# Kernel tuning notes

Hardware: AMD Instinct MI355X
Metric: run time of the kernel (lower is better)

## Reference

```python
import jax, jax.numpy as jnp
import numpy as np


def setup_inputs() -> dict:
    key = jax.random.key(0)
    ka, kb = jax.random.split(key)
    a = jax.random.normal(ka, (8, 2048, 1024), dtype=jnp.float32)
    b = jax.random.normal(kb, (8, 2048, 1024), dtype=jnp.float32)
    return {"a": a, "b": b}


def reference(a, b):
    # e[b,i,j] = <a_i, b_j>
    e = jnp.einsum("bid,bjd->bij", a, b)  # [B, La, Lb]
    e_b = jax.nn.softmax(e, axis=2)        # softmax over b-tokens
    e_a = jax.nn.softmax(e, axis=1)        # softmax over a-tokens
    a_tilda = jnp.einsum("bij,bjd->bid", e_b, b)  # [B, La, D]
    b_tilda = jnp.einsum("bij,bid->bjd", e_a, a)  # [B, Lb, D]
    return (a_tilda, b_tilda)
```

## Files before the change

kernel.cpp:

```cpp
#include <hip/hip_runtime.h>

#define BATCH 8
#define L 2048
#define D 1024

#define PB_OFF  (L * L)
#define PAT_OFF (L * L + (L * L) / 2)
#define STAT    (2 * L * L)
#define ROWINV  0
#define CMAXP   (L)
#define CMAX    (17 * L)
#define CSUMP   (18 * L)
#define CINV    (26 * L)
#define SLOT_F  (2 * L * L + 28 * L)

typedef __attribute__((ext_vector_type(8))) short bf16x8;
typedef __attribute__((ext_vector_type(4))) float f32x4;

static __device__ inline unsigned short f2bf(float x) {
  union { float f; unsigned u; } v; v.f = x;
  unsigned r = v.u + 0x7fff + ((v.u >> 16) & 1);
  return (unsigned short)(r >> 16);
}
static __device__ inline float bf2f(unsigned short h) {
  union { unsigned u; float f; } v; v.u = ((unsigned)h) << 16; return v.f;
}
static __device__ inline unsigned pack2(float x, float y) {
  return (unsigned)f2bf(x) | ((unsigned)f2bf(y) << 16);
}
static __device__ inline void split2(float x, float y, unsigned &hi, unsigned &lo) {
  unsigned short hx = f2bf(x), hy = f2bf(y);
  float rx = x - bf2f(hx), ry = y - bf2f(hy);
  hi = (unsigned)hx | ((unsigned)hy << 16);
  lo = (unsigned)f2bf(rx) | ((unsigned)f2bf(ry) << 16);
}

#define GLL16(gp, lp) __builtin_amdgcn_global_load_lds(                        \
    (const __attribute__((address_space(1))) void*)(gp),                       \
    (__attribute__((address_space(3))) void*)(lp), 16, 0, 0)

static __device__ inline void stage2(const unsigned short* __restrict__ g,
                                     size_t o0, size_t o1,
                                     unsigned short* l, int wb) {
  GLL16(g + o0, l + wb);
  GLL16(g + o1, l + wb + 2048);
}

__global__ __launch_bounds__(256) void k_prep(const float* __restrict__ A,
                                              const float* __restrict__ Bm,
                                              unsigned short* __restrict__ at,
                                              unsigned short* __restrict__ bt,
                                              unsigned short* __restrict__ ah,
                                              unsigned short* __restrict__ al,
                                              unsigned short* __restrict__ bh,
                                              unsigned short* __restrict__ bl) {
  const int z = blockIdx.z, batch = z & 7;
  const bool isA = z < 8;
  const float* src = (isA ? A : Bm) + (size_t)batch * L * D;
  unsigned short* dst = (isA ? at : bt) + (size_t)batch * D * L;
  unsigned short* ph = (isA ? ah : bh) + (size_t)batch * L * D;
  unsigned short* pl = (isA ? al : bl) + (size_t)batch * L * D;
  const int i0 = blockIdx.x * 64, d0 = blockIdx.y * 64;
  __shared__ float sT[64][65];
  const int tid = threadIdx.x;
#pragma unroll
  for (int it = 0; it < 4; ++it) {
    int idx = tid + it * 256;
    int row = idx >> 4, c4 = (idx & 15) * 4;
    float4 v = *(const float4*)(src + (size_t)(i0 + row) * D + d0 + c4);
    unsigned h0, l0, h1, l1;
    split2(v.x, v.y, h0, l0); split2(v.z, v.w, h1, l1);
    size_t po = (size_t)(i0 + row) * D + d0 + c4;
    *(uint2*)&ph[po] = make_uint2(h0, h1);
    *(uint2*)&pl[po] = make_uint2(l0, l1);
    sT[row][c4 + 0] = v.x; sT[row][c4 + 1] = v.y;
    sT[row][c4 + 2] = v.z; sT[row][c4 + 3] = v.w;
  }
  __syncthreads();
#pragma unroll
  for (int it = 0; it < 4; ++it) {
    int idx = tid + it * 256;
    int orow = idx >> 4, c4 = (idx & 15) * 4;
    uint2 o = make_uint2(pack2(sT[c4 + 0][orow], sT[c4 + 1][orow]),
                         pack2(sT[c4 + 2][orow], sT[c4 + 3][orow]));
    *(uint2*)&dst[(size_t)(d0 + orow) * L + i0 + c4] = o;
  }
}

__global__ __launch_bounds__(256) void k_gemm_e(const unsigned short* __restrict__ ah,
                                                const unsigned short* __restrict__ al,
                                                const unsigned short* __restrict__ bh,
                                                const unsigned short* __restrict__ bl,
                                                float* __restrict__ ws, int b0) {
  const int bz = blockIdx.z, batch = b0 + bz;
  const size_t po = (size_t)batch * L * D;
  float* e = ws + (size_t)bz * SLOT_F;
  const int i0 = blockIdx.x * 128, j0 = blockIdx.y * 128;
  __shared__ unsigned short sAh[128 * 32], sAl[128 * 32];
  __shared__ unsigned short sBh[128 * 32], sBl[128 * 32];
  const int tid = threadIdx.x, lane = tid & 63, wave = tid >> 6;
  const int wm = (wave & 1) * 64, wn = (wave >> 1) * 64;
  const int q = lane >> 4, lr = lane & 15;
  const int soff = wave * 1024 + lane * 16;
  const int srow = soff >> 6, scol = (soff & 63) >> 1;
  const int wb = wave * 512;
  const unsigned short* gAh = ah + po; const unsigned short* gAl = al + po;
  const unsigned short* gBh = bh + po; const unsigned short* gBl = bl + po;
  const size_t ga0 = (size_t)(i0 + srow) * D + scol, ga1 = ga0 + (size_t)64 * D;
  const size_t gb0 = (size_t)(j0 + srow) * D + scol, gb1 = gb0 + (size_t)64 * D;
  f32x4 acc[4][4] = {};
  for (int k0 = 0; k0 < D; k0 += 32) {
    __syncthreads();
    stage2(gAh, ga0 + k0, ga1 + k0, sAh, wb);
    stage2(gAl, ga0 + k0, ga1 + k0, sAl, wb);
    stage2(gBh, gb0 + k0, gb1 + k0, sBh, wb);
    stage2(gBl, gb0 + k0, gb1 + k0, sBl, wb);
    __syncthreads();
    bf16x8 fah[4], fbh[4], fx[4];
#pragma unroll
    for (int t = 0; t < 4; ++t) {
      fah[t] = *(const bf16x8*)&sAh[(wm + t * 16 + lr) * 32 + q * 8];
      fbh[t] = *(const bf16x8*)&sBh[(wn + t * 16 + lr) * 32 + q * 8];
    }
#pragma unroll
    for (int mi = 0; mi < 4; ++mi)
#pragma unroll
      for (int ni = 0; ni < 4; ++ni)
        acc[mi][ni] = __builtin_amdgcn_mfma_f32_16x16x32_bf16(fah[mi], fbh[ni], acc[mi][ni], 0, 0, 0);
#pragma unroll
    for (int t = 0; t < 4; ++t)
      fx[t] = *(const bf16x8*)&sBl[(wn + t * 16 + lr) * 32 + q * 8];
#pragma unroll
    for (int mi = 0; mi < 4; ++mi)
#pragma unroll
      for (int ni = 0; ni < 4; ++ni)
        acc[mi][ni] = __builtin_amdgcn_mfma_f32_16x16x32_bf16(fah[mi], fx[ni], acc[mi][ni], 0, 0, 0);
#pragma unroll
    for (int t = 0; t < 4; ++t)
      fx[t] = *(const bf16x8*)&sAl[(wm + t * 16 + lr) * 32 + q * 8];
#pragma unroll
    for (int mi = 0; mi < 4; ++mi)
#pragma unroll
      for (int ni = 0; ni < 4; ++ni)
        acc[mi][ni] = __builtin_amdgcn_mfma_f32_16x16x32_bf16(fx[mi], fbh[ni], acc[mi][ni], 0, 0, 0);
  }
#pragma unroll
  for (int mi = 0; mi < 4; ++mi)
#pragma unroll
    for (int ni = 0; ni < 4; ++ni)
#pragma unroll
      for (int r = 0; r < 4; ++r)
        e[(size_t)(i0 + wm + mi * 16 + q * 4 + r) * L + (j0 + wn + ni * 16 + lr)] =
            acc[mi][ni][r];
}

__global__ __launch_bounds__(256) void k_rowsoft(float* __restrict__ ws) {
  float* slot = ws + (size_t)blockIdx.y * SLOT_F;
  const int row = blockIdx.x, tid = threadIdx.x;
  const float* er = slot + (size_t)row * L;
  float v[8]; float m = -INFINITY;
#pragma unroll
  for (int r = 0; r < 8; ++r) { v[r] = er[tid + r * 256]; m = fmaxf(m, v[r]); }
  __shared__ float red[4];
#pragma unroll
  for (int o = 32; o; o >>= 1) m = fmaxf(m, __shfl_xor(m, o));
  if ((tid & 63) == 0) red[tid >> 6] = m;
  __syncthreads();
  m = fmaxf(fmaxf(red[0], red[1]), fmaxf(red[2], red[3]));
  float ex[8], s = 0.f;
#pragma unroll
  for (int r = 0; r < 8; ++r) { ex[r] = __expf(v[r] - m); s += ex[r]; }
  __syncthreads();
#pragma unroll
  for (int o = 32; o; o >>= 1) s += __shfl_xor(s, o);
  if ((tid & 63) == 0) red[tid >> 6] = s;
  __syncthreads();
  unsigned short* P = (unsigned short*)(slot + PB_OFF) + (size_t)row * L;
#pragma unroll
  for (int r = 0; r < 8; ++r) P[tid + r * 256] = f2bf(ex[r]);
  if (tid == 0)
    slot[STAT + ROWINV + row] = 1.0f / (red[0] + red[1] + red[2] + red[3]);
}

__global__ __launch_bounds__(256) void k_colmax(float* __restrict__ ws) {
  float* slot = ws + (size_t)blockIdx.z * SLOT_F;
  const float* e = slot;
  float* st = slot + STAT;
  const int j0 = blockIdx.x * 64, i0 = blockIdx.y * 256;
  const int tid = threadIdx.x;
  const int rr = tid >> 4, c4 = (tid & 15) * 4;
  float m0 = -INFINITY, m1 = -INFINITY, m2 = -INFINITY, m3 = -INFINITY;
#pragma unroll 4
  for (int i = rr; i < 256; i += 16) {
    float4 v = *(const float4*)(e + (size_t)(i0 + i) * L + j0 + c4);
    m0 = fmaxf(m0, v.x); m1 = fmaxf(m1, v.y);
    m2 = fmaxf(m2, v.z); m3 = fmaxf(m3, v.w);
  }
  __shared__ float red[16][64];
  red[rr][c4 + 0] = m0; red[rr][c4 + 1] = m1;
  red[rr][c4 + 2] = m2; red[rr][c4 + 3] = m3;
  __syncthreads();
  if (tid < 64) {
    float m = red[0][tid];
#pragma unroll
    for (int g = 1; g < 16; ++g) m = fmaxf(m, red[g][tid]);
    st[CMAXP + (size_t)blockIdx.y * L + j0 + tid] = m;
  }
}

__global__ __launch_bounds__(256) void k_colstat2(float* __restrict__ ws) {
  float* st = ws + (size_t)blockIdx.y * SLOT_F + STAT;
  const int j = blockIdx.x * 256 + threadIdx.x;
  float m = st[CMAXP + j];
#pragma unroll
  for (int k = 1; k < 8; ++k) m = fmaxf(m, st[CMAXP + (size_t)k * L + j]);
  st[CMAX + j] = m;
}

__global__ __launch_bounds__(256) void k_colexp(float* __restrict__ ws) {
  float* slot = ws + (size_t)blockIdx.z * SLOT_F;
  const float* e = slot;
  float* st = slot + STAT;
  const int j0 = blockIdx.x * 64, i0 = blockIdx.y * 256;
  const int tid = threadIdx.x;
  const int rr = tid >> 4, c4 = (tid & 15) * 4;
  __shared__ unsigned short sT[64][72];
  __shared__ float psumL[16][64];
  float cm[4], ps[4] = {0.f, 0.f, 0.f, 0.f};
#pragma unroll
  for (int k = 0; k < 4; ++k) cm[k] = st[CMAX + j0 + c4 + k];
  unsigned short* PaT = (unsigned short*)(slot + PAT_OFF);
  for (int sub = 0; sub < 4; ++sub) {
    const int ib = i0 + sub * 64;
    __syncthreads();
#pragma unroll
    for (int p = 0; p < 4; ++p) {
      const int r = rr + p * 16;
      float4 v = *(const float4*)(e + (size_t)(ib + r) * L + j0 + c4);
      float e0 = __expf(v.x - cm[0]), e1 = __expf(v.y - cm[1]);
      float e2 = __expf(v.z - cm[2]), e3 = __expf(v.w - cm[3]);
      ps[0] += e0; ps[1] += e1; ps[2] += e2; ps[3] += e3;
      sT[c4 + 0][r] = f2bf(e0); sT[c4 + 1][r] = f2bf(e1);
      sT[c4 + 2][r] = f2bf(e2); sT[c4 + 3][r] = f2bf(e3);
    }
    __syncthreads();
    const int cc = tid >> 2, qd = tid & 3;
    uint4 o0 = *(const uint4*)&sT[cc][qd * 8];
    uint4 o1 = *(const uint4*)&sT[cc][32 + qd * 8];
    *(uint4*)&PaT[(size_t)(j0 + cc) * L + ib + qd * 8] = o0;
    *(uint4*)&PaT[(size_t)(j0 + cc) * L + ib + 32 + qd * 8] = o1;
  }
  psumL[rr][c4 + 0] = ps[0]; psumL[rr][c4 + 1] = ps[1];
  psumL[rr][c4 + 2] = ps[2]; psumL[rr][c4 + 3] = ps[3];
  __syncthreads();
  if (tid < 64) {
    float s = 0.f;
#pragma unroll
    for (int g = 0; g < 16; ++g) s += psumL[g][tid];
    st[CSUMP + (size_t)blockIdx.y * L + j0 + tid] = s;
  }
}

__global__ __launch_bounds__(256) void k_colfin(float* __restrict__ ws) {
  float* st = ws + (size_t)blockIdx.y * SLOT_F + STAT;
  const int j = blockIdx.x * 256 + threadIdx.x;
  float s = 0.f;
#pragma unroll
  for (int k = 0; k < 8; ++k) s += st[CSUMP + (size_t)k * L + j];
  st[CINV + j] = 1.0f / s;
}

__global__ __launch_bounds__(256) void k_pv(const unsigned short* __restrict__ at,
                                            const unsigned short* __restrict__ bt,
                                            float* __restrict__ ws,
                                            float* __restrict__ outB,
                                            int b0, int nb) {
  const int z = blockIdx.z;
  const int pair = (z >= nb) ? 1 : 0;
  const int bz = z - pair * nb;
  const int batch = b0 + bz;
  float* slot = ws + (size_t)bz * SLOT_F;
  const unsigned short* P =
      (const unsigned short*)(slot + (pair ? PAT_OFF : PB_OFF));
  const unsigned short* W = (pair ? at : bt) + (size_t)batch * D * L;
  float* out = outB + (size_t)(pair * BATCH + batch) * L * D;
  const float* sc = slot + STAT + (pair ? CINV : ROWINV);
  const int m0 = blockIdx.x * 128, d0 = blockIdx.y * 128;
  __shared__ unsigned short sP[128 * 64], sW[128 * 64];
  const int tid = threadIdx.x, lane = tid & 63, wave = tid >> 6;
  const int wm = (wave & 1) * 64, wn = (wave >> 1) * 64;
  const int q = lane >> 4, lr = lane & 15;
  const int srow = wave * 8 + (lane >> 3);
  const int scolu = ((lane & 7) ^ (lane >> 3)) * 8;
  const size_t gp = (size_t)(m0 + srow) * L + scolu;
  const size_t gw = (size_t)(d0 + srow) * L + scolu;
  const int ldsb = wave * 512;
  const int swz = (lr & 7) << 3;
  f32x4 acc[4][4] = {};
  for (int k0 = 0; k0 < L; k0 += 64) {
    __syncthreads();
#pragma unroll
    for (int it = 0; it < 4; ++it) {
      GLL16(P + gp + (size_t)it * 32 * L + k0, sP + ldsb + it * 2048);
      GLL16(W + gw + (size_t)it * 32 * L + k0, sW + ldsb + it * 2048);
    }
    __syncthreads();
#pragma unroll
    for (int kk = 0; kk < 2; ++kk) {
      bf16x8 fa[4], fb[4];
#pragma unroll
      for (int t = 0; t < 4; ++t) {
        fa[t] = *(const bf16x8*)&sP[(wm + t * 16 + lr) * 64 + ((kk * 32 + q * 8) ^ swz)];
        fb[t] = *(const bf16x8*)&sW[(wn + t * 16 + lr) * 64 + ((kk * 32 + q * 8) ^ swz)];
      }
#pragma unroll
      for (int mi = 0; mi < 4; ++mi)
#pragma unroll
        for (int ni = 0; ni < 4; ++ni)
          acc[mi][ni] = __builtin_amdgcn_mfma_f32_16x16x32_bf16(fa[mi], fb[ni], acc[mi][ni], 0, 0, 0);
    }
  }
  float rsc[4][4];
#pragma unroll
  for (int mi = 0; mi < 4; ++mi)
#pragma unroll
    for (int r = 0; r < 4; ++r)
      rsc[mi][r] = sc[m0 + wm + mi * 16 + q * 4 + r];
#pragma unroll
  for (int mi = 0; mi < 4; ++mi)
#pragma unroll
    for (int ni = 0; ni < 4; ++ni)
#pragma unroll
      for (int r = 0; r < 4; ++r)
        out[(size_t)(m0 + wm + mi * 16 + q * 4 + r) * D + (d0 + wn + ni * 16 + lr)] =
            acc[mi][ni][r] * rsc[mi][r];
}

extern "C" void kernel_launch(void* const* d_in, const int* in_sizes, int n_in,
                              void* d_out, int out_size, void* d_ws, size_t ws_size,
                              hipStream_t stream) {
  const float* a = (const float*)d_in[0];
  const float* b = (const float*)d_in[1];
  float* out = (float*)d_out;
  const size_t PL = (size_t)BATCH * D * L;
  unsigned short* at = (unsigned short*)d_ws;
  unsigned short* bt = at + PL;
  unsigned short* ah = bt + PL;
  unsigned short* al = ah + PL;
  unsigned short* bh = al + PL;
  unsigned short* bl = bh + PL;
  float* slots = (float*)(bl + PL);
  const size_t base_bytes = 6 * PL * sizeof(unsigned short);
  const size_t slot_bytes = (size_t)SLOT_F * sizeof(float);
  int S = 1;
  if (ws_size > base_bytes + slot_bytes)
    S = (int)((ws_size - base_bytes) / slot_bytes);
  if (S > BATCH) S = BATCH;
  if (S < 1) S = 1;

  hipLaunchKernelGGL(k_prep, dim3(L / 64, D / 64, 2 * BATCH), dim3(256), 0, stream,
                     a, b, at, bt, ah, al, bh, bl);
  for (int b0 = 0; b0 < BATCH; b0 += S) {
    int nb = (BATCH - b0 < S) ? (BATCH - b0) : S;
    hipLaunchKernelGGL(k_gemm_e, dim3(16, 16, nb), dim3(256), 0, stream,
                       ah, al, bh, bl, slots, b0);
    hipLaunchKernelGGL(k_rowsoft, dim3(L, nb), dim3(256), 0, stream, slots);
    hipLaunchKernelGGL(k_colmax, dim3(L / 64, L / 256, nb), dim3(256), 0, stream, slots);
    hipLaunchKernelGGL(k_colstat2, dim3(L / 256, nb), dim3(256), 0, stream, slots);
    hipLaunchKernelGGL(k_colexp, dim3(L / 64, L / 256, nb), dim3(256), 0, stream, slots);
    hipLaunchKernelGGL(k_colfin, dim3(L / 256, nb), dim3(256), 0, stream, slots);
    hipLaunchKernelGGL(k_pv, dim3(16, 8, 2 * nb), dim3(256), 0, stream,
                       at, bt, slots, out, b0, nb);
  }
}
```

Measured before the change: 720.5 us.

## Fold column-stat reductions into consumers and double-buffer PV LDS tiles

```diff
diff --git a/kernel.cpp b/kernel.cpp
--- a/kernel.cpp
+++ b/kernel.cpp
@@ -9,9 +9,7 @@
 #define STAT    (2 * L * L)
 #define ROWINV  0
 #define CMAXP   (L)
-#define CMAX    (17 * L)
 #define CSUMP   (18 * L)
-#define CINV    (26 * L)
 #define SLOT_F  (2 * L * L + 28 * L)
 
 typedef __attribute__((ext_vector_type(8))) short bf16x8;
@@ -208,15 +206,6 @@
   }
 }
 
-__global__ __launch_bounds__(256) void k_colstat2(float* __restrict__ ws) {
-  float* st = ws + (size_t)blockIdx.y * SLOT_F + STAT;
-  const int j = blockIdx.x * 256 + threadIdx.x;
-  float m = st[CMAXP + j];
-#pragma unroll
-  for (int k = 1; k < 8; ++k) m = fmaxf(m, st[CMAXP + (size_t)k * L + j]);
-  st[CMAX + j] = m;
-}
-
 __global__ __launch_bounds__(256) void k_colexp(float* __restrict__ ws) {
   float* slot = ws + (size_t)blockIdx.z * SLOT_F;
   const float* e = slot;
@@ -228,7 +217,13 @@
   __shared__ float psumL[16][64];
   float cm[4], ps[4] = {0.f, 0.f, 0.f, 0.f};
 #pragma unroll
-  for (int k = 0; k < 4; ++k) cm[k] = st[CMAX + j0 + c4 + k];
+  for (int k = 0; k < 4; ++k) {
+    float m = st[CMAXP + j0 + c4 + k];
+#pragma unroll
+    for (int p = 1; p < 8; ++p)
+      m = fmaxf(m, st[CMAXP + (size_t)p * L + j0 + c4 + k]);
+    cm[k] = m;
+  }
   unsigned short* PaT = (unsigned short*)(slot + PAT_OFF);
   for (int sub = 0; sub < 4; ++sub) {
     const int ib = i0 + sub * 64;
@@ -259,15 +254,6 @@
     for (int g = 0; g < 16; ++g) s += psumL[g][tid];
     st[CSUMP + (size_t)blockIdx.y * L + j0 + tid] = s;
   }
-}
-
-__global__ __launch_bounds__(256) void k_colfin(float* __restrict__ ws) {
-  float* st = ws + (size_t)blockIdx.y * SLOT_F + STAT;
-  const int j = blockIdx.x * 256 + threadIdx.x;
-  float s = 0.f;
-#pragma unroll
-  for (int k = 0; k < 8; ++k) s += st[CSUMP + (size_t)k * L + j];
-  st[CINV + j] = 1.0f / s;
 }
 
 __global__ __launch_bounds__(256) void k_pv(const unsigned short* __restrict__ at,
@@ -284,9 +270,10 @@
       (const unsigned short*)(slot + (pair ? PAT_OFF : PB_OFF));
   const unsigned short* W = (pair ? at : bt) + (size_t)batch * D * L;
   float* out = outB + (size_t)(pair * BATCH + batch) * L * D;
-  const float* sc = slot + STAT + (pair ? CINV : ROWINV);
+  const float* st = slot + STAT;
   const int m0 = blockIdx.x * 128, d0 = blockIdx.y * 128;
-  __shared__ unsigned short sP[128 * 64], sW[128 * 64];
+  __shared__ unsigned short sP0[128 * 64], sP1[128 * 64];
+  __shared__ unsigned short sW0[128 * 64], sW1[128 * 64];
   const int tid = threadIdx.x, lane = tid & 63, wave = tid >> 6;
   const int wm = (wave & 1) * 64, wn = (wave >> 1) * 64;
   const int q = lane >> 4, lr = lane & 15;
@@ -297,35 +284,58 @@
   const int ldsb = wave * 512;
   const int swz = (lr & 7) << 3;
   f32x4 acc[4][4] = {};
+#pragma unroll
+  for (int it = 0; it < 4; ++it) {
+    GLL16(P + gp + (size_t)it * 32 * L, sP0 + ldsb + it * 2048);
+    GLL16(W + gw + (size_t)it * 32 * L, sW0 + ldsb + it * 2048);
+  }
+  __syncthreads();
+  int cur = 0;
   for (int k0 = 0; k0 < L; k0 += 64) {
-    __syncthreads();
-#pragma unroll
-    for (int it = 0; it < 4; ++it) {
-      GLL16(P + gp + (size_t)it * 32 * L + k0, sP + ldsb + it * 2048);
-      GLL16(W + gw + (size_t)it * 32 * L + k0, sW + ldsb + it * 2048);
+    unsigned short* bpP = cur ? sP1 : sP0;
+    unsigned short* bpW = cur ? sW1 : sW0;
+    unsigned short* bnP = cur ? sP0 : sP1;
+    unsigned short* bnW = cur ? sW0 : sW1;
+    bf16x8 fa[2][4], fb[2][4];
+#pragma unroll
+    for (int kk = 0; kk < 2; ++kk)
+#pragma unroll
+      for (int t = 0; t < 4; ++t) {
+        fa[kk][t] = *(const bf16x8*)&bpP[(wm + t * 16 + lr) * 64 + ((kk * 32 + q * 8) ^ swz)];
+        fb[kk][t] = *(const bf16x8*)&bpW[(wn + t * 16 + lr) * 64 + ((kk * 32 + q * 8) ^ swz)];
+      }
+    if (k0 + 64 < L) {
+#pragma unroll
+      for (int it = 0; it < 4; ++it) {
+        GLL16(P + gp + (size_t)it * 32 * L + k0 + 64, bnP + ldsb + it * 2048);
+        GLL16(W + gw + (size_t)it * 32 * L + k0 + 64, bnW + ldsb + it * 2048);
+      }
     }
-    __syncthreads();
-#pragma unroll
-    for (int kk = 0; kk < 2; ++kk) {
-      bf16x8 fa[4], fb[4];
-#pragma unroll
-      for (int t = 0; t < 4; ++t) {
-        fa[t] = *(const bf16x8*)&sP[(wm + t * 16 + lr) * 64 + ((kk * 32 + q * 8) ^ swz)];
-        fb[t] = *(const bf16x8*)&sW[(wn + t * 16 + lr) * 64 + ((kk * 32 + q * 8) ^ swz)];
+#pragma unroll
+    for (int kk = 0; kk < 2; ++kk)
+#pragma unroll
+      for (int mi = 0; mi < 4; ++mi)
+#pragma unroll
+        for (int ni = 0; ni < 4; ++ni)
+          acc[mi][ni] = __builtin_amdgcn_mfma_f32_16x16x32_bf16(fa[kk][mi], fb[kk][ni], acc[mi][ni], 0, 0, 0);
+    __syncthreads();
+    cur ^= 1;
+  }
+  float rsc[4][4];
+#pragma unroll
+  for (int mi = 0; mi < 4; ++mi)
+#pragma unroll
+    for (int r = 0; r < 4; ++r) {
+      const int row = m0 + wm + mi * 16 + q * 4 + r;
+      if (pair) {
+        float s = 0.f;
+#pragma unroll
+        for (int k = 0; k < 8; ++k) s += st[CSUMP + (size_t)k * L + row];
+        rsc[mi][r] = 1.0f / s;
+      } else {
+        rsc[mi][r] = st[ROWINV + row];
       }
-#pragma unroll
-      for (int mi = 0; mi < 4; ++mi)
-#pragma unroll
-        for (int ni = 0; ni < 4; ++ni)
-          acc[mi][ni] = __builtin_amdgcn_mfma_f32_16x16x32_bf16(fa[mi], fb[ni], acc[mi][ni], 0, 0, 0);
     }
-  }
-  float rsc[4][4];
-#pragma unroll
-  for (int mi = 0; mi < 4; ++mi)
-#pragma unroll
-    for (int r = 0; r < 4; ++r)
-      rsc[mi][r] = sc[m0 + wm + mi * 16 + q * 4 + r];
 #pragma unroll
   for (int mi = 0; mi < 4; ++mi)
 #pragma unroll
@@ -366,9 +376,7 @@
                        ah, al, bh, bl, slots, b0);
     hipLaunchKernelGGL(k_rowsoft, dim3(L, nb), dim3(256), 0, stream, slots);
     hipLaunchKernelGGL(k_colmax, dim3(L / 64, L / 256, nb), dim3(256), 0, stream, slots);
-    hipLaunchKernelGGL(k_colstat2, dim3(L / 256, nb), dim3(256), 0, stream, slots);
     hipLaunchKernelGGL(k_colexp, dim3(L / 64, L / 256, nb), dim3(256), 0, stream, slots);
-    hipLaunchKernelGGL(k_colfin, dim3(L / 256, nb), dim3(256), 0, stream, slots);
     hipLaunchKernelGGL(k_pv, dim3(16, 8, 2 * nb), dim3(256), 0, stream,
                        at, bt, slots, out, b0, nb);
   }
```

Result: no change. 718.1 us (-0.3%).
